# Optimization experiments

Hardware: AMD Instinct MI355X
Metric: run time of the kernel (lower is better)

## Reference

```python
import jax, jax.numpy as jnp
import numpy as np

EMBED_DIM = 1024
NUM_HEADS = 16
HEAD_DIM = EMBED_DIM // NUM_HEADS


def setup_inputs() -> dict:
    key = jax.random.key(0)
    k1, k2, k3, k4, k5 = jax.random.split(key, 5)
    B, N, C = 8, 1024, EMBED_DIM
    s = 1.0 / np.sqrt(C)
    return {
        "x": jax.random.normal(k1, (B, N, C), dtype=jnp.float32),
        "in_proj_weight": jax.random.normal(k2, (3 * C, C), dtype=jnp.float32) * s,
        "in_proj_bias": jax.random.normal(k3, (3 * C,), dtype=jnp.float32) * 0.02,
        "out_proj_weight": jax.random.normal(k4, (C, C), dtype=jnp.float32) * s,
        "out_proj_bias": jax.random.normal(k5, (C,), dtype=jnp.float32) * 0.02,
    }


def reference(x, in_proj_weight, in_proj_bias, out_proj_weight, out_proj_bias):
    B, N, C = x.shape
    scale = HEAD_DIM ** -0.5
    # qkv projection: F.linear(x, W, b) = x @ W.T + b -> [B, N, 3C]
    qkv = jnp.einsum("bnc,dc->bnd", x, in_proj_weight) + in_proj_bias
    # [B, N, 3, H, Dh] -> [3, B, H, N, Dh]
    qkv = qkv.reshape(B, N, 3, NUM_HEADS, HEAD_DIM).transpose(2, 0, 3, 1, 4)
    q, k, v = qkv[0], qkv[1], qkv[2]
    attn = jnp.einsum("bhqd,bhkd->bhqk", q, k) * scale
    attn = jax.nn.softmax(attn, axis=-1)
    out = jnp.einsum("bhqk,bhkd->bhqd", attn, v)
    out = out.transpose(0, 2, 1, 3).reshape(B, N, C)
    return jnp.einsum("bnc,dc->bnd", out, out_proj_weight) + out_proj_bias
```

## Files before the change

### kernel.cpp

```cpp
#include <hip/hip_runtime.h>
#include <math.h>
#include <stdint.h>

#define SEQ   1024
#define BATCH 8
#define CDIM  1024
#define HEADS 16
#define DHEAD 64

typedef __bf16 bf16;
typedef _Float16 f16;
typedef __attribute__((ext_vector_type(8))) __bf16 bf16x8;
typedef __attribute__((ext_vector_type(8))) _Float16 f16x8;
typedef __attribute__((ext_vector_type(4))) float f32x4;

static __device__ __forceinline__ void gl16(const void* g, void* l) {
    __builtin_amdgcn_global_load_lds(
        (const __attribute__((address_space(1))) void*)(uintptr_t)g,
        (__attribute__((address_space(3))) void*)(uintptr_t)l,
        16, 0, 0);
}

__global__ __launch_bounds__(256)
void cvt_f16(const float* __restrict__ in, f16* __restrict__ out, int n8)
{
    int i = blockIdx.x * blockDim.x + threadIdx.x;
    const int stride = gridDim.x * blockDim.x;
    for (; i < n8; i += stride) {
        const f32x4 v0 = *(const f32x4*)(in + (size_t)i * 8);
        const f32x4 v1 = *(const f32x4*)(in + (size_t)i * 8 + 4);
        f16x8 o;
#pragma unroll
        for (int j = 0; j < 4; j++) {
            o[j]     = (f16)v0[j];
            o[j + 4] = (f16)v1[j];
        }
        *(f16x8*)(out + (size_t)i * 8) = o;
    }
}

template<int MODE>
__global__ __launch_bounds__(256, 4)
void gemm_f16(const f16* __restrict__ Ag, const f16* __restrict__ Bg,
              const float* __restrict__ bias, float* __restrict__ out0,
              f16* __restrict__ qg, f16* __restrict__ kgp, f16* __restrict__ vgp,
              int M, int Ncols, int K)
{
    __shared__ f16 As[4][128][8];
    __shared__ f16 Bs[4][128][8];

    const int tid  = threadIdx.x;
    const int m0   = blockIdx.y * 128;
    const int n0   = blockIdx.x * 128;
    const int wid  = tid >> 6;
    const int lane = tid & 63;
    const int wr   = (wid >> 1) * 64;
    const int wc   = (wid & 1) * 64;
    const int l16  = lane & 15;
    const int kgf  = lane >> 4;

    const int kg0 = tid >> 7, row0 = tid & 127;

    const f16* aP = Ag + (size_t)(m0 + row0) * K + kg0 * 8;
    const f16* bP = Bg + (size_t)(n0 + row0) * K + kg0 * 8;

    char* ldsA = (char*)&As[0][0][0] + (wid << 10);
    char* ldsB = (char*)&Bs[0][0][0] + (wid << 10);

    f32x4 acc[4][4];
#pragma unroll
    for (int i = 0; i < 4; i++)
#pragma unroll
        for (int j = 0; j < 4; j++) acc[i][j] = (f32x4)0.f;

    for (int kt = 0; kt < K; kt += 32) {
        __syncthreads();
        gl16(aP + kt,      ldsA);
        gl16(aP + kt + 16, ldsA + 4096);
        gl16(bP + kt,      ldsB);
        gl16(bP + kt + 16, ldsB + 4096);
        __syncthreads();

        f16x8 fa[4], fb[4];
#pragma unroll
        for (int i = 0; i < 4; i++) {
            fa[i] = *(const f16x8*)&As[kgf][wr + i * 16 + l16][0];
            fb[i] = *(const f16x8*)&Bs[kgf][wc + i * 16 + l16][0];
        }
#pragma unroll
        for (int mi = 0; mi < 4; mi++)
#pragma unroll
            for (int ni = 0; ni < 4; ni++)
                acc[mi][ni] = __builtin_amdgcn_mfma_f32_16x16x32_f16(
                    fa[mi], fb[ni], acc[mi][ni], 0, 0, 0);
    }

#pragma unroll
    for (int ni = 0; ni < 4; ni++) {
        const int d  = n0 + wc + ni * 16 + l16;
        const float bv = bias[d];
        int s = 0, hh = 0, dh = 0;
        if (MODE == 1) {
            s  = d >> 10;
            hh = (d >> 6) & 15;
            dh = d & 63;
        }
#pragma unroll
        for (int mi = 0; mi < 4; mi++) {
            const int mbase = m0 + wr + mi * 16 + (lane >> 4) * 4;
#pragma unroll
            for (int r = 0; r < 4; r++) {
                const float v = acc[mi][ni][r] + bv;
                const int m = mbase + r;
                if (MODE == 0) {
                    out0[(size_t)m * Ncols + d] = v;
                } else {
                    const int b = m >> 10, n = m & 1023;
                    const size_t bho = (size_t)((b << 4) + hh) << 16;
                    if (s == 0)
                        qg[bho + ((size_t)n << 6) + dh] = (f16)(v * 0.125f);
                    else if (s == 1)
                        kgp[bho + ((size_t)n << 6) + dh] = (f16)v;
                    else
                        vgp[bho + ((size_t)dh << 10) + n] = (f16)v;
                }
            }
        }
    }
    (void)M;
}

__global__ __launch_bounds__(256, 4)
void attn_mfma(const f16* __restrict__ qf, const f16* __restrict__ kf,
               const f16* __restrict__ vtf, f16* __restrict__ og)
{
    __shared__ f16 Kl[8][64][8];
    __shared__ f16 Vl[8][64][8];
    __shared__ f16 Pl[4][16][72];

    const int tid  = threadIdx.x;
    const int wid  = tid >> 6;
    const int lane = tid & 63;
    const int l16  = lane & 15;
    const int kg   = lane >> 4;
    const int bh   = blockIdx.y;
    const int q0   = blockIdx.x << 6;

    const size_t bhoff = (size_t)bh << 16;
    const f16* qb = qf  + bhoff;
    const f16* kb = kf  + bhoff;
    const f16* vb = vtf + bhoff;

    f16x8 qfr[2];
    {
        const f16* qrow = qb + ((size_t)(q0 + wid * 16 + l16) << 6);
        qfr[0] = *(const f16x8*)(qrow + kg * 8);
        qfr[1] = *(const f16x8*)(qrow + 32 + kg * 8);
    }

    const int c0 = tid,        col0 = c0 & 63, slot0 = c0 >> 6;
    const int c1 = tid + 256,  col1 = c1 & 63, slot1 = c1 >> 6;

    float mrow[4], lrow[4];
    f32x4 accO[4];
#pragma unroll
    for (int r = 0; r < 4; r++) { mrow[r] = -INFINITY; lrow[r] = 0.f; }
#pragma unroll
    for (int t = 0; t < 4; t++) accO[t] = (f32x4)0.f;

    f16x8 rk0 = *(const f16x8*)(kb + ((size_t)col0 << 6) + slot0 * 8);
    f16x8 rk1 = *(const f16x8*)(kb + ((size_t)col1 << 6) + slot1 * 8);
    f16x8 rv0 = *(const f16x8*)(vb + ((size_t)col0 << 10) + slot0 * 8);
    f16x8 rv1 = *(const f16x8*)(vb + ((size_t)col1 << 10) + slot1 * 8);

    for (int kt = 0; kt < 16; kt++) {
        __syncthreads();
        *(f16x8*)&Kl[slot0][col0][0] = rk0;
        *(f16x8*)&Kl[slot1][col1][0] = rk1;
        *(f16x8*)&Vl[slot0][col0][0] = rv0;
        *(f16x8*)&Vl[slot1][col1][0] = rv1;
        __syncthreads();

        if (kt < 15) {
            const int n1 = (kt + 1) << 6;
            rk0 = *(const f16x8*)(kb + ((size_t)(n1 + col0) << 6) + slot0 * 8);
            rk1 = *(const f16x8*)(kb + ((size_t)(n1 + col1) << 6) + slot1 * 8);
            rv0 = *(const f16x8*)(vb + ((size_t)col0 << 10) + n1 + slot0 * 8);
            rv1 = *(const f16x8*)(vb + ((size_t)col1 << 10) + n1 + slot1 * 8);
        }

        f32x4 accS[4];
#pragma unroll
        for (int t = 0; t < 4; t++) accS[t] = (f32x4)0.f;
#pragma unroll
        for (int t = 0; t < 4; t++) {
            const f16x8 kf0 = *(const f16x8*)&Kl[kg][t * 16 + l16][0];
            const f16x8 kf1 = *(const f16x8*)&Kl[4 + kg][t * 16 + l16][0];
            accS[t] = __builtin_amdgcn_mfma_f32_16x16x32_f16(qfr[0], kf0, accS[t], 0, 0, 0);
            accS[t] = __builtin_amdgcn_mfma_f32_16x16x32_f16(qfr[1], kf1, accS[t], 0, 0, 0);
        }

#pragma unroll
        for (int r = 0; r < 4; r++) {
            float sm = fmaxf(fmaxf(accS[0][r], accS[1][r]),
                             fmaxf(accS[2][r], accS[3][r]));
            sm = fmaxf(sm, __shfl_xor(sm, 1, 16));
            sm = fmaxf(sm, __shfl_xor(sm, 2, 16));
            sm = fmaxf(sm, __shfl_xor(sm, 4, 16));
            sm = fmaxf(sm, __shfl_xor(sm, 8, 16));
            const float mn = fmaxf(mrow[r], sm);
            const float al = __expf(mrow[r] - mn);
            float p0 = __expf(accS[0][r] - mn);
            float p1 = __expf(accS[1][r] - mn);
            float p2 = __expf(accS[2][r] - mn);
            float p3 = __expf(accS[3][r] - mn);
            float rs = (p0 + p1) + (p2 + p3);
            rs += __shfl_xor(rs, 1, 16);
            rs += __shfl_xor(rs, 2, 16);
            rs += __shfl_xor(rs, 4, 16);
            rs += __shfl_xor(rs, 8, 16);
            lrow[r] = lrow[r] * al + rs;
            mrow[r] = mn;
            accO[0][r] *= al;
            accO[1][r] *= al;
            accO[2][r] *= al;
            accO[3][r] *= al;
            const int prow = kg * 4 + r;
            Pl[wid][prow][l16]      = (f16)p0;
            Pl[wid][prow][16 + l16] = (f16)p1;
            Pl[wid][prow][32 + l16] = (f16)p2;
            Pl[wid][prow][48 + l16] = (f16)p3;
        }

#pragma unroll
        for (int h = 0; h < 2; h++) {
            const f16x8 pa = *(const f16x8*)&Pl[wid][l16][h * 32 + kg * 8];
#pragma unroll
            for (int t = 0; t < 4; t++) {
                const f16x8 vf = *(const f16x8*)&Vl[h * 4 + kg][t * 16 + l16][0];
                accO[t] = __builtin_amdgcn_mfma_f32_16x16x32_f16(pa, vf, accO[t], 0, 0, 0);
            }
        }
    }

    const int b = bh >> 4, hh = bh & 15;
#pragma unroll
    for (int r = 0; r < 4; r++) {
        const float inv = 1.0f / lrow[r];
        const int n = q0 + wid * 16 + kg * 4 + r;
        const size_t base = ((((size_t)b << 10) + n) << 10) + hh * 64;
#pragma unroll
        for (int t = 0; t < 4; t++)
            og[base + t * 16 + l16] = (f16)(accO[t][r] * inv);
    }
}

#define TILE 128
#define KB   16
#define LSTR (TILE + 4)

template<int MODE>
__global__ __launch_bounds__(256, 2)
void gemm_bt(const float* __restrict__ A, const float* __restrict__ Bm,
             const float* __restrict__ bias, float* __restrict__ out0,
             float* __restrict__ qg, float* __restrict__ kg, float* __restrict__ vg,
             int M, int Ncols, int K)
{
    __shared__ float As[KB][LSTR];
    __shared__ float Bs[KB][LSTR];

    const int tid = threadIdx.x;
    const int tr  = tid >> 4;
    const int tc  = tid & 15;
    const int m0  = blockIdx.y * TILE;
    const int n0  = blockIdx.x * TILE;

    const int lrow = tid >> 2;
    const int lcol = (tid & 3) << 2;

    const float* Ap = A  + (size_t)(m0 + lrow) * K + lcol;
    const float* Bp = Bm + (size_t)(n0 + lrow) * K + lcol;
    const size_t rstep = (size_t)64 * K;

    float acc[8][8];
#pragma unroll
    for (int i = 0; i < 8; i++)
#pragma unroll
        for (int j = 0; j < 8; j++) acc[i][j] = 0.f;

    for (int kt = 0; kt < K; kt += KB) {
        float4 a0 = *(const float4*)(Ap + kt);
        float4 a1 = *(const float4*)(Ap + rstep + kt);
        float4 b0 = *(const float4*)(Bp + kt);
        float4 b1 = *(const float4*)(Bp + rstep + kt);
        __syncthreads();
        As[lcol + 0][lrow]      = a0.x;
        As[lcol + 1][lrow]      = a0.y;
        As[lcol + 2][lrow]      = a0.z;
        As[lcol + 3][lrow]      = a0.w;
        As[lcol + 0][lrow + 64] = a1.x;
        As[lcol + 1][lrow + 64] = a1.y;
        As[lcol + 2][lrow + 64] = a1.z;
        As[lcol + 3][lrow + 64] = a1.w;
        Bs[lcol + 0][lrow]      = b0.x;
        Bs[lcol + 1][lrow]      = b0.y;
        Bs[lcol + 2][lrow]      = b0.z;
        Bs[lcol + 3][lrow]      = b0.w;
        Bs[lcol + 0][lrow + 64] = b1.x;
        Bs[lcol + 1][lrow + 64] = b1.y;
        Bs[lcol + 2][lrow + 64] = b1.z;
        Bs[lcol + 3][lrow + 64] = b1.w;
        __syncthreads();
#pragma unroll
        for (int kk = 0; kk < KB; kk++) {
            float ar[8], br[8];
            *(float4*)&ar[0] = *(const float4*)&As[kk][tr << 2];
            *(float4*)&ar[4] = *(const float4*)&As[kk][64 + (tr << 2)];
            *(float4*)&br[0] = *(const float4*)&Bs[kk][tc << 2];
            *(float4*)&br[4] = *(const float4*)&Bs[kk][64 + (tc << 2)];
#pragma unroll
            for (int i = 0; i < 8; i++)
#pragma unroll
                for (int j = 0; j < 8; j++)
                    acc[i][j] = fmaf(ar[i], br[j], acc[i][j]);
        }
    }

#pragma unroll
    for (int rg = 0; rg < 2; rg++) {
#pragma unroll
        for (int ri = 0; ri < 4; ri++) {
            const int m = m0 + rg * 64 + (tr << 2) + ri;
#pragma unroll
            for (int cg = 0; cg < 2; cg++) {
                const int d = n0 + cg * 64 + (tc << 2);
                const float4 bb = *(const float4*)&bias[d];
                float v0 = acc[rg * 4 + ri][cg * 4 + 0] + bb.x;
                float v1 = acc[rg * 4 + ri][cg * 4 + 1] + bb.y;
                float v2 = acc[rg * 4 + ri][cg * 4 + 2] + bb.z;
                float v3 = acc[rg * 4 + ri][cg * 4 + 3] + bb.w;
                if (MODE == 0) {
                    *(float4*)&out0[(size_t)m * Ncols + d] = make_float4(v0, v1, v2, v3);
                } else {
                    const int s  = d >> 10;
                    const int h  = (d >> 6) & 15;
                    const int dh = d & 63;
                    const int b  = m >> 10;
                    const int n  = m & 1023;
                    float* dst = (s == 0) ? qg : ((s == 1) ? kg : vg);
                    if (s == 0) { v0 *= 0.125f; v1 *= 0.125f; v2 *= 0.125f; v3 *= 0.125f; }
                    const size_t idx = (((size_t)((b << 4) + h) << 10) + n) * 64 + dh;
                    *(float4*)&dst[idx] = make_float4(v0, v1, v2, v3);
                }
            }
        }
    }
}

__global__ __launch_bounds__(256, 2)
void attn_flash_f32(const float* __restrict__ qg, const float* __restrict__ kg,
                    const float* __restrict__ vg, float* __restrict__ og)
{
    __shared__ float Qs[64][68];
    __shared__ float KPs[64][68];
    __shared__ float Vs[64][68];

    const int tid = threadIdx.x;
    const int tr  = tid >> 4;
    const int tc  = tid & 15;
    const int bh  = blockIdx.y;
    const int q0  = blockIdx.x << 6;

    const float* qb = qg + ((size_t)bh * SEQ + q0) * DHEAD;
    const float* kb = kg + (size_t)bh * SEQ * DHEAD;
    const float* vb = vg + (size_t)bh * SEQ * DHEAD;

    const int lr = tid >> 4;
    const int lc = (tid & 15) << 2;

#pragma unroll
    for (int i = 0; i < 4; i++) {
        const int r = lr + (i << 4);
        float4 t = *(const float4*)(qb + r * 64 + lc);
        Qs[lc + 0][r] = t.x;
        Qs[lc + 1][r] = t.y;
        Qs[lc + 2][r] = t.z;
        Qs[lc + 3][r] = t.w;
    }

    float m[4], l[4], acc[4][4];
#pragma unroll
    for (int i = 0; i < 4; i++) {
        m[i] = -INFINITY; l[i] = 0.f;
#pragma unroll
        for (int j = 0; j < 4; j++) acc[i][j] = 0.f;
    }

    for (int kt = 0; kt < 16; kt++) {
        __syncthreads();
        const float* kbt = kb + (size_t)(kt << 6) * 64;
        const float* vbt = vb + (size_t)(kt << 6) * 64;
#pragma unroll
        for (int i = 0; i < 4; i++) {
            const int r = lr + (i << 4);
            float4 t = *(const float4*)(kbt + r * 64 + lc);
            KPs[lc + 0][r] = t.x;
            KPs[lc + 1][r] = t.y;
            KPs[lc + 2][r] = t.z;
            KPs[lc + 3][r] = t.w;
            float4 tv = *(const float4*)(vbt + r * 64 + lc);
            *(float4*)&Vs[r][lc] = tv;
        }
        __syncthreads();

        float s[4][4];
#pragma unroll
        for (int i = 0; i < 4; i++)
#pragma unroll
            for (int j = 0; j < 4; j++) s[i][j] = 0.f;
#pragma unroll 4
        for (int d = 0; d < 64; d++) {
            float qa[4], ka[4];
            *(float4*)qa = *(const float4*)&Qs[d][tr << 2];
            *(float4*)ka = *(const float4*)&KPs[d][tc << 2];
#pragma unroll
            for (int ri = 0; ri < 4; ri++)
#pragma unroll
                for (int ci = 0; ci < 4; ci++)
                    s[ri][ci] = fmaf(qa[ri], ka[ci], s[ri][ci]);
        }
        __syncthreads();

#pragma unroll
        for (int ri = 0; ri < 4; ri++) {
            float tm = fmaxf(fmaxf(s[ri][0], s[ri][1]), fmaxf(s[ri][2], s[ri][3]));
            tm = fmaxf(tm, __shfl_xor(tm, 1, 16));
            tm = fmaxf(tm, __shfl_xor(tm, 2, 16));
            tm = fmaxf(tm, __shfl_xor(tm, 4, 16));
            tm = fmaxf(tm, __shfl_xor(tm, 8, 16));
            const float mn = fmaxf(m[ri], tm);
            const float alpha = __expf(m[ri] - mn);
            const float p0 = __expf(s[ri][0] - mn);
            const float p1 = __expf(s[ri][1] - mn);
            const float p2 = __expf(s[ri][2] - mn);
            const float p3 = __expf(s[ri][3] - mn);
            float rs = (p0 + p1) + (p2 + p3);
            rs += __shfl_xor(rs, 1, 16);
            rs += __shfl_xor(rs, 2, 16);
            rs += __shfl_xor(rs, 4, 16);
            rs += __shfl_xor(rs, 8, 16);
            l[ri] = l[ri] * alpha + rs;
            m[ri] = mn;
            acc[ri][0] *= alpha; acc[ri][1] *= alpha;
            acc[ri][2] *= alpha; acc[ri][3] *= alpha;
            *(float4*)&KPs[(tr << 2) + ri][tc << 2] = make_float4(p0, p1, p2, p3);
        }
        __syncthreads();

#pragma unroll 4
        for (int c = 0; c < 64; c += 4) {
            float pr[4][4], vv[4][4];
            *(float4*)pr[0] = *(const float4*)&KPs[(tr << 2) + 0][c];
            *(float4*)pr[1] = *(const float4*)&KPs[(tr << 2) + 1][c];
            *(float4*)pr[2] = *(const float4*)&KPs[(tr << 2) + 2][c];
            *(float4*)pr[3] = *(const float4*)&KPs[(tr << 2) + 3][c];
            *(float4*)vv[0] = *(const float4*)&Vs[c + 0][tc << 2];
            *(float4*)vv[1] = *(const float4*)&Vs[c + 1][tc << 2];
            *(float4*)vv[2] = *(const float4*)&Vs[c + 2][tc << 2];
            *(float4*)vv[3] = *(const float4*)&Vs[c + 3][tc << 2];
#pragma unroll
            for (int ri = 0; ri < 4; ri++)
#pragma unroll
                for (int j = 0; j < 4; j++) {
                    float a = acc[ri][j];
                    a = fmaf(pr[ri][0], vv[0][j], a);
                    a = fmaf(pr[ri][1], vv[1][j], a);
                    a = fmaf(pr[ri][2], vv[2][j], a);
                    a = fmaf(pr[ri][3], vv[3][j], a);
                    acc[ri][j] = a;
                }
        }
    }

    const int b = bh >> 4, h = bh & 15;
#pragma unroll
    for (int ri = 0; ri < 4; ri++) {
        const float inv = 1.0f / l[ri];
        const int n = q0 + (tr << 2) + ri;
        const size_t idx = (((size_t)b * SEQ + n) << 10) + (h << 6) + (tc << 2);
        *(float4*)&og[idx] = make_float4(acc[ri][0] * inv, acc[ri][1] * inv,
                                         acc[ri][2] * inv, acc[ri][3] * inv);
    }
}

extern "C" void kernel_launch(void* const* d_in, const int* in_sizes, int n_in,
                              void* d_out, int out_size, void* d_ws, size_t ws_size,
                              hipStream_t stream)
{
    const float* x     = (const float*)d_in[0];
    const float* w_in  = (const float*)d_in[1];
    const float* b_in  = (const float*)d_in[2];
    const float* w_out = (const float*)d_in[3];
    const float* b_out = (const float*)d_in[4];
    float* out = (float*)d_out;
    (void)in_sizes; (void)n_in; (void)out_size;

    const size_t MB  = 1024 * 1024;
    const size_t per = (size_t)BATCH * HEADS * SEQ * DHEAD;
    const int    M   = BATCH * SEQ;
    char* ws = (char*)d_ws;

    if (ws_size >= 96 * MB) {
        f16* qf16  = (f16*)(ws + 0 * MB);
        f16* kf16  = (f16*)(ws + 16 * MB);
        f16* vtf16 = (f16*)(ws + 32 * MB);
        f16* xf16  = (f16*)(ws + 48 * MB);
        f16* of16  = xf16;
        f16* wif16 = (f16*)(ws + 64 * MB);
        f16* wof16 = (f16*)(ws + 70 * MB);

        cvt_f16<<<2048, 256, 0, stream>>>(x,     xf16,  (int)(per / 8));
        cvt_f16<<<1024, 256, 0, stream>>>(w_in,  wif16, 3 * CDIM * CDIM / 8);
        cvt_f16<<<512,  256, 0, stream>>>(w_out, wof16, CDIM * CDIM / 8);

        gemm_f16<1><<<dim3(3 * CDIM / 128, M / 128), 256, 0, stream>>>(
            xf16, wif16, b_in, nullptr, qf16, kf16, vtf16, M, 3 * CDIM, CDIM);

        attn_mfma<<<dim3(SEQ / 64, BATCH * HEADS), 256, 0, stream>>>(
            qf16, kf16, vtf16, of16);

        gemm_f16<0><<<dim3(CDIM / 128, M / 128), 256, 0, stream>>>(
            of16, wof16, b_out, out, nullptr, nullptr, nullptr, M, CDIM, CDIM);
    } else {
        float* qws = (float*)d_ws;
        float* kws = qws + per;
        float* vws = kws + per;
        float* aws = vws + per;

        gemm_bt<1><<<dim3(3 * CDIM / TILE, M / TILE), 256, 0, stream>>>(
            x, w_in, b_in, nullptr, qws, kws, vws, M, 3 * CDIM, CDIM);

        attn_flash_f32<<<dim3(SEQ / 64, BATCH * HEADS), 256, 0, stream>>>(
            qws, kws, vws, aws);

        gemm_bt<0><<<dim3(CDIM / TILE, M / TILE), 256, 0, stream>>>(
            aws, w_out, b_out, out, nullptr, nullptr, nullptr, M, CDIM, CDIM);
    }
}
```

Before: 289.0 us.

## Double-buffer GEMM LDS tiles and swizzle workgroup order for L2 locality

Splits the GEMM shared-memory tiles into two buffers so the global-to-LDS loads for the next K step are issued while MFMAs run on the current one, dropping one barrier per iteration. It also remaps the linear workgroup index in groups of eight so neighbouring workgroups share A/B rows in cache. LDS use per block doubles, which may limit occupancy under launch_bounds(256,4), and the swizzle assumes the workgroup count is divisible by eight.

```diff
diff --git a/kernel.cpp b/kernel.cpp
--- a/kernel.cpp
+++ b/kernel.cpp
@@ -10,7 +10,6 @@
 
 typedef __bf16 bf16;
 typedef _Float16 f16;
-typedef __attribute__((ext_vector_type(8))) __bf16 bf16x8;
 typedef __attribute__((ext_vector_type(8))) _Float16 f16x8;
 typedef __attribute__((ext_vector_type(4))) float f32x4;
 
@@ -46,12 +45,18 @@
               f16* __restrict__ qg, f16* __restrict__ kgp, f16* __restrict__ vgp,
               int M, int Ncols, int K)
 {
-    __shared__ f16 As[4][128][8];
-    __shared__ f16 Bs[4][128][8];
+    __shared__ f16 As[2][4][128][8];
+    __shared__ f16 Bs[2][4][128][8];
+
+    const int nx   = gridDim.x;
+    const int nwg  = nx * gridDim.y;
+    const int lin  = blockIdx.y * nx + blockIdx.x;
+    const int cpx  = nwg >> 3;
+    const int swz  = (lin & 7) * cpx + (lin >> 3);
+    const int m0   = (swz / nx) * 128;
+    const int n0   = (swz % nx) * 128;
 
     const int tid  = threadIdx.x;
-    const int m0   = blockIdx.y * 128;
-    const int n0   = blockIdx.x * 128;
     const int wid  = tid >> 6;
     const int lane = tid & 63;
     const int wr   = (wid >> 1) * 64;
@@ -60,12 +65,9 @@
     const int kgf  = lane >> 4;
 
     const int kg0 = tid >> 7, row0 = tid & 127;
-
     const f16* aP = Ag + (size_t)(m0 + row0) * K + kg0 * 8;
     const f16* bP = Bg + (size_t)(n0 + row0) * K + kg0 * 8;
-
-    char* ldsA = (char*)&As[0][0][0] + (wid << 10);
-    char* ldsB = (char*)&Bs[0][0][0] + (wid << 10);
+    const int loff = wid << 10;
 
     f32x4 acc[4][4];
 #pragma unroll
@@ -73,19 +75,29 @@
 #pragma unroll
         for (int j = 0; j < 4; j++) acc[i][j] = (f32x4)0.f;
 
-    for (int kt = 0; kt < K; kt += 32) {
-        __syncthreads();
-        gl16(aP + kt,      ldsA);
-        gl16(aP + kt + 16, ldsA + 4096);
-        gl16(bP + kt,      ldsB);
-        gl16(bP + kt + 16, ldsB + 4096);
-        __syncthreads();
+    gl16(aP,      (char*)&As[0][0][0][0] + loff);
+    gl16(aP + 16, (char*)&As[0][0][0][0] + loff + 4096);
+    gl16(bP,      (char*)&Bs[0][0][0][0] + loff);
+    gl16(bP + 16, (char*)&Bs[0][0][0][0] + loff + 4096);
+    __syncthreads();
+
+    const int T = K >> 5;
+    for (int t = 0; t < T; t++) {
+        const int cur = t & 1;
+        if (t + 1 < T) {
+            const int nxt = cur ^ 1;
+            const int kn  = (t + 1) << 5;
+            gl16(aP + kn,      (char*)&As[nxt][0][0][0] + loff);
+            gl16(aP + kn + 16, (char*)&As[nxt][0][0][0] + loff + 4096);
+            gl16(bP + kn,      (char*)&Bs[nxt][0][0][0] + loff);
+            gl16(bP + kn + 16, (char*)&Bs[nxt][0][0][0] + loff + 4096);
+        }
 
         f16x8 fa[4], fb[4];
 #pragma unroll
         for (int i = 0; i < 4; i++) {
-            fa[i] = *(const f16x8*)&As[kgf][wr + i * 16 + l16][0];
-            fb[i] = *(const f16x8*)&Bs[kgf][wc + i * 16 + l16][0];
+            fa[i] = *(const f16x8*)&As[cur][kgf][wr + i * 16 + l16][0];
+            fb[i] = *(const f16x8*)&Bs[cur][kgf][wc + i * 16 + l16][0];
         }
 #pragma unroll
         for (int mi = 0; mi < 4; mi++)
@@ -93,6 +105,8 @@
             for (int ni = 0; ni < 4; ni++)
                 acc[mi][ni] = __builtin_amdgcn_mfma_f32_16x16x32_f16(
                     fa[mi], fb[ni], acc[mi][ni], 0, 0, 0);
+
+        __syncthreads();
     }
 
 #pragma unroll
```

After: 285.4 us. About the same (-1.2%).

## Triple-buffer GEMM LDS tiles with async prefetch two stages ahead

Applied to the files above, without the earlier changes.

Replaces the single-buffer load-sync-compute loop in the f16 GEMM with a three-stage LDS ring. Direct global-to-LDS loads are issued two K-tiles ahead, and explicit vmcnt waits plus barriers gate each compute step. The goal is to hide global memory latency behind the MFMA work instead of stalling on every tile. In exchange, LDS per block triples, and the occupancy hint drops from 4 to 3 blocks per CU.

```diff
diff --git a/kernel.cpp b/kernel.cpp
--- a/kernel.cpp
+++ b/kernel.cpp
@@ -10,7 +10,6 @@
 
 typedef __bf16 bf16;
 typedef _Float16 f16;
-typedef __attribute__((ext_vector_type(8))) __bf16 bf16x8;
 typedef __attribute__((ext_vector_type(8))) _Float16 f16x8;
 typedef __attribute__((ext_vector_type(4))) float f32x4;
 
@@ -40,18 +39,19 @@
 }
 
 template<int MODE>
-__global__ __launch_bounds__(256, 4)
+__global__ __launch_bounds__(256, 3)
 void gemm_f16(const f16* __restrict__ Ag, const f16* __restrict__ Bg,
               const float* __restrict__ bias, float* __restrict__ out0,
               f16* __restrict__ qg, f16* __restrict__ kgp, f16* __restrict__ vgp,
               int M, int Ncols, int K)
 {
-    __shared__ f16 As[4][128][8];
-    __shared__ f16 Bs[4][128][8];
-
-    const int tid  = threadIdx.x;
+    __shared__ f16 As[3][4][128][8];
+    __shared__ f16 Bs[3][4][128][8];
+
     const int m0   = blockIdx.y * 128;
     const int n0   = blockIdx.x * 128;
+
+    const int tid  = threadIdx.x;
     const int wid  = tid >> 6;
     const int lane = tid & 63;
     const int wr   = (wid >> 1) * 64;
@@ -60,12 +60,33 @@
     const int kgf  = lane >> 4;
 
     const int kg0 = tid >> 7, row0 = tid & 127;
-
     const f16* aP = Ag + (size_t)(m0 + row0) * K + kg0 * 8;
     const f16* bP = Bg + (size_t)(n0 + row0) * K + kg0 * 8;
-
-    char* ldsA = (char*)&As[0][0][0] + (wid << 10);
-    char* ldsB = (char*)&Bs[0][0][0] + (wid << 10);
+    const int loff = wid << 10;
+
+#define STAGE(buf, kt)                                              \
+    do {                                                            \
+        gl16(aP + (kt),      (char*)&As[buf][0][0][0] + loff);      \
+        gl16(aP + (kt) + 16, (char*)&As[buf][0][0][0] + loff + 4096);\
+        gl16(bP + (kt),      (char*)&Bs[buf][0][0][0] + loff);      \
+        gl16(bP + (kt) + 16, (char*)&Bs[buf][0][0][0] + loff + 4096);\
+    } while (0)
+
+#define COMPUTE(buf)                                                        \
+    do {                                                                    \
+        f16x8 fa[4], fb[4];                                                 \
+        _Pragma("unroll")                                                   \
+        for (int i = 0; i < 4; i++) {                                       \
+            fa[i] = *(const f16x8*)&As[buf][kgf][wr + i * 16 + l16][0];     \
+            fb[i] = *(const f16x8*)&Bs[buf][kgf][wc + i * 16 + l16][0];     \
+        }                                                                   \
+        _Pragma("unroll")                                                   \
+        for (int mi = 0; mi < 4; mi++)                                      \
+            _Pragma("unroll")                                               \
+            for (int ni = 0; ni < 4; ni++)                                  \
+                acc[mi][ni] = __builtin_amdgcn_mfma_f32_16x16x32_f16(       \
+                    fa[mi], fb[ni], acc[mi][ni], 0, 0, 0);                  \
+    } while (0)
 
     f32x4 acc[4][4];
 #pragma unroll
@@ -73,27 +94,42 @@
 #pragma unroll
         for (int j = 0; j < 4; j++) acc[i][j] = (f32x4)0.f;
 
-    for (int kt = 0; kt < K; kt += 32) {
-        __syncthreads();
-        gl16(aP + kt,      ldsA);
-        gl16(aP + kt + 16, ldsA + 4096);
-        gl16(bP + kt,      ldsB);
-        gl16(bP + kt + 16, ldsB + 4096);
-        __syncthreads();
-
-        f16x8 fa[4], fb[4];
-#pragma unroll
-        for (int i = 0; i < 4; i++) {
-            fa[i] = *(const f16x8*)&As[kgf][wr + i * 16 + l16][0];
-            fb[i] = *(const f16x8*)&Bs[kgf][wc + i * 16 + l16][0];
-        }
-#pragma unroll
-        for (int mi = 0; mi < 4; mi++)
-#pragma unroll
-            for (int ni = 0; ni < 4; ni++)
-                acc[mi][ni] = __builtin_amdgcn_mfma_f32_16x16x32_f16(
-                    fa[mi], fb[ni], acc[mi][ni], 0, 0, 0);
-    }
+    const int T = K >> 5;
+
+    STAGE(0, 0);
+    STAGE(1, 32);
+
+    int cur = 0;
+    for (int t = 0; t < T - 2; t++) {
+        const int nbuf = (cur == 0) ? 2 : (cur - 1);
+        STAGE(nbuf, (t + 2) << 5);
+        asm volatile("s_waitcnt vmcnt(8)" ::: "memory");
+        __builtin_amdgcn_sched_barrier(0);
+        __builtin_amdgcn_s_barrier();
+        __builtin_amdgcn_sched_barrier(0);
+        COMPUTE(cur);
+        __builtin_amdgcn_sched_barrier(0);
+        __builtin_amdgcn_s_barrier();
+        cur = (cur == 2) ? 0 : (cur + 1);
+    }
+
+    asm volatile("s_waitcnt vmcnt(4)" ::: "memory");
+    __builtin_amdgcn_sched_barrier(0);
+    __builtin_amdgcn_s_barrier();
+    __builtin_amdgcn_sched_barrier(0);
+    COMPUTE(cur);
+    __builtin_amdgcn_sched_barrier(0);
+    __builtin_amdgcn_s_barrier();
+    cur = (cur == 2) ? 0 : (cur + 1);
+
+    asm volatile("s_waitcnt vmcnt(0)" ::: "memory");
+    __builtin_amdgcn_sched_barrier(0);
+    __builtin_amdgcn_s_barrier();
+    __builtin_amdgcn_sched_barrier(0);
+    COMPUTE(cur);
+
+#undef STAGE
+#undef COMPUTE
 
 #pragma unroll
     for (int ni = 0; ni < 4; ni++) {
```

Measured after the change: 286.9 us. About the same (-0.7%).

## Double-buffer GEMM with 128x256 tiles and merge conversion kernels

Applied to the files above, without the earlier changes.

The GEMM now uses 128x256 output tiles per block, so each wave computes a 64x128 sub-tile. The K-loop prefetches the next K-slice into a second LDS buffer with async global-to-LDS loads and waits only on the older loads before computing. The three fp32-to-fp16 conversion launches become one kernel. This cuts the per-iteration load-latency stall and launch overhead. In exchange it uses more registers and LDS, with occupancy lowered to 3 waves, and the output projection now runs only 256 blocks, which may underfill the GPU.

```diff
diff --git a/kernel.cpp b/kernel.cpp
--- a/kernel.cpp
+++ b/kernel.cpp
@@ -10,7 +10,6 @@
 
 typedef __bf16 bf16;
 typedef _Float16 f16;
-typedef __attribute__((ext_vector_type(8))) __bf16 bf16x8;
 typedef __attribute__((ext_vector_type(8))) _Float16 f16x8;
 typedef __attribute__((ext_vector_type(4))) float f32x4;
 
@@ -22,82 +21,117 @@
 }
 
 __global__ __launch_bounds__(256)
-void cvt_f16(const float* __restrict__ in, f16* __restrict__ out, int n8)
+void cvt_all(const float* __restrict__ x,  const float* __restrict__ wi,
+             const float* __restrict__ wo, f16* __restrict__ xo,
+             f16* __restrict__ wio, f16* __restrict__ woo)
 {
+    const int N1 = 1048576, N2 = 393216;
+    const int NT = N1 + N2 + 131072;
     int i = blockIdx.x * blockDim.x + threadIdx.x;
     const int stride = gridDim.x * blockDim.x;
-    for (; i < n8; i += stride) {
-        const f32x4 v0 = *(const f32x4*)(in + (size_t)i * 8);
-        const f32x4 v1 = *(const f32x4*)(in + (size_t)i * 8 + 4);
+    for (; i < NT; i += stride) {
+        const float* src; f16* dst; int off;
+        if (i < N1)            { src = x;  dst = xo;  off = i; }
+        else if (i < N1 + N2)  { src = wi; dst = wio; off = i - N1; }
+        else                   { src = wo; dst = woo; off = i - N1 - N2; }
+        const f32x4 v0 = *(const f32x4*)(src + (size_t)off * 8);
+        const f32x4 v1 = *(const f32x4*)(src + (size_t)off * 8 + 4);
         f16x8 o;
 #pragma unroll
         for (int j = 0; j < 4; j++) {
             o[j]     = (f16)v0[j];
             o[j + 4] = (f16)v1[j];
         }
-        *(f16x8*)(out + (size_t)i * 8) = o;
+        *(f16x8*)(dst + (size_t)off * 8) = o;
     }
 }
 
 template<int MODE>
-__global__ __launch_bounds__(256, 4)
-void gemm_f16(const f16* __restrict__ Ag, const f16* __restrict__ Bg,
-              const float* __restrict__ bias, float* __restrict__ out0,
-              f16* __restrict__ qg, f16* __restrict__ kgp, f16* __restrict__ vgp,
-              int M, int Ncols, int K)
+__global__ __launch_bounds__(256, 3)
+void gemm_wide(const f16* __restrict__ Ag, const f16* __restrict__ Bg,
+               const float* __restrict__ bias, float* __restrict__ out0,
+               f16* __restrict__ qg, f16* __restrict__ kgp,
+               f16* __restrict__ vgp, int Ncols, int K)
 {
-    __shared__ f16 As[4][128][8];
-    __shared__ f16 Bs[4][128][8];
+    __shared__ f16 As[2][4][128][8];
+    __shared__ f16 Bs[2][4][256][8];
+
+    const int m0 = blockIdx.y * 128;
+    const int n0 = blockIdx.x * 256;
 
     const int tid  = threadIdx.x;
-    const int m0   = blockIdx.y * 128;
-    const int n0   = blockIdx.x * 128;
     const int wid  = tid >> 6;
     const int lane = tid & 63;
     const int wr   = (wid >> 1) * 64;
-    const int wc   = (wid & 1) * 64;
+    const int wc   = (wid & 1) * 128;
     const int l16  = lane & 15;
     const int kgf  = lane >> 4;
 
-    const int kg0 = tid >> 7, row0 = tid & 127;
-
-    const f16* aP = Ag + (size_t)(m0 + row0) * K + kg0 * 8;
-    const f16* bP = Bg + (size_t)(n0 + row0) * K + kg0 * 8;
-
-    char* ldsA = (char*)&As[0][0][0] + (wid << 10);
-    char* ldsB = (char*)&Bs[0][0][0] + (wid << 10);
-
-    f32x4 acc[4][4];
+    const int akg = tid >> 7, arow = tid & 127;
+    const f16* aP = Ag + (size_t)(m0 + arow) * K + akg * 8;
+    const f16* bP = Bg + (size_t)(n0 + tid) * K;
+    const int loff = wid << 10;
+
+#define STAGE(buf, kt)                                               \
+    do {                                                             \
+        gl16(aP + (kt),      (char*)As[buf] + loff);                 \
+        gl16(aP + (kt) + 16, (char*)As[buf] + loff + 4096);          \
+        gl16(bP + (kt),      (char*)Bs[buf] + loff);                 \
+        gl16(bP + (kt) + 8,  (char*)Bs[buf] + loff + 4096);         \
+        gl16(bP + (kt) + 16, (char*)Bs[buf] + loff + 8192);         \
+        gl16(bP + (kt) + 24, (char*)Bs[buf] + loff + 12288);        \
+    } while (0)
+
+#define COMPUTE(buf)                                                         \
+    do {                                                                     \
+        f16x8 fa[4], fb[8];                                                  \
+        _Pragma("unroll")                                                    \
+        for (int i = 0; i < 4; i++)                                          \
+            fa[i] = *(const f16x8*)&As[buf][kgf][wr + i * 16 + l16][0];      \
+        _Pragma("unroll")                                                    \
+        for (int j = 0; j < 8; j++)                                          \
+            fb[j] = *(const f16x8*)&Bs[buf][kgf][wc + j * 16 + l16][0];      \
+        _Pragma("unroll")                                                    \
+        for (int i = 0; i < 4; i++)                                          \
+            _Pragma("unroll")                                                \
+            for (int j = 0; j < 8; j++)                                      \
+                acc[i][j] = __builtin_amdgcn_mfma_f32_16x16x32_f16(          \
+                    fa[i], fb[j], acc[i][j], 0, 0, 0);                       \
+    } while (0)
+
+    f32x4 acc[4][8];
 #pragma unroll
     for (int i = 0; i < 4; i++)
 #pragma unroll
-        for (int j = 0; j < 4; j++) acc[i][j] = (f32x4)0.f;
-
-    for (int kt = 0; kt < K; kt += 32) {
-        __syncthreads();
-        gl16(aP + kt,      ldsA);
-        gl16(aP + kt + 16, ldsA + 4096);
-        gl16(bP + kt,      ldsB);
-        gl16(bP + kt + 16, ldsB + 4096);
-        __syncthreads();
-
-        f16x8 fa[4], fb[4];
-#pragma unroll
-        for (int i = 0; i < 4; i++) {
-            fa[i] = *(const f16x8*)&As[kgf][wr + i * 16 + l16][0];
-            fb[i] = *(const f16x8*)&Bs[kgf][wc + i * 16 + l16][0];
-        }
-#pragma unroll
-        for (int mi = 0; mi < 4; mi++)
-#pragma unroll
-            for (int ni = 0; ni < 4; ni++)
-                acc[mi][ni] = __builtin_amdgcn_mfma_f32_16x16x32_f16(
-                    fa[mi], fb[ni], acc[mi][ni], 0, 0, 0);
-    }
-
-#pragma unroll
-    for (int ni = 0; ni < 4; ni++) {
-        const int d  = n0 + wc + ni * 16 + l16;
+        for (int j = 0; j < 8; j++) acc[i][j] = (f32x4)0.f;
+
+    const int T = K >> 5;
+
+    STAGE(0, 0);
+
+    int cur = 0;
+    for (int t = 0; t < T; t++) {
+        if (t + 1 < T) {
+            STAGE(cur ^ 1, (t + 1) << 5);
+            asm volatile("s_waitcnt vmcnt(6)" ::: "memory");
+        } else {
+            asm volatile("s_waitcnt vmcnt(0)" ::: "memory");
+        }
+        __builtin_amdgcn_sched_barrier(0);
+        __builtin_amdgcn_s_barrier();
+        __builtin_amdgcn_sched_barrier(0);
+        COMPUTE(cur);
+        __builtin_amdgcn_sched_barrier(0);
+        __builtin_amdgcn_s_barrier();
+        cur ^= 1;
+    }
+
+#undef STAGE
+#undef COMPUTE
+
+#pragma unroll
+    for (int j = 0; j < 8; j++) {
+        const int d  = n0 + wc + j * 16 + l16;
         const float bv = bias[d];
         int s = 0, hh = 0, dh = 0;
         if (MODE == 1) {
@@ -106,11 +140,11 @@
             dh = d & 63;
         }
 #pragma unroll
-        for (int mi = 0; mi < 4; mi++) {
-            const int mbase = m0 + wr + mi * 16 + (lane >> 4) * 4;
+        for (int i = 0; i < 4; i++) {
+            const int mbase = m0 + wr + i * 16 + (lane >> 4) * 4;
 #pragma unroll
             for (int r = 0; r < 4; r++) {
-                const float v = acc[mi][ni][r] + bv;
+                const float v = acc[i][j][r] + bv;
                 const int m = mbase + r;
                 if (MODE == 0) {
                     out0[(size_t)m * Ncols + d] = v;
@@ -127,7 +161,6 @@
             }
         }
     }
-    (void)M;
 }
 
 __global__ __launch_bounds__(256, 4)
@@ -519,18 +552,16 @@
         f16* wif16 = (f16*)(ws + 64 * MB);
         f16* wof16 = (f16*)(ws + 70 * MB);
 
-        cvt_f16<<<2048, 256, 0, stream>>>(x,     xf16,  (int)(per / 8));
-        cvt_f16<<<1024, 256, 0, stream>>>(w_in,  wif16, 3 * CDIM * CDIM / 8);
-        cvt_f16<<<512,  256, 0, stream>>>(w_out, wof16, CDIM * CDIM / 8);
-
-        gemm_f16<1><<<dim3(3 * CDIM / 128, M / 128), 256, 0, stream>>>(
-            xf16, wif16, b_in, nullptr, qf16, kf16, vtf16, M, 3 * CDIM, CDIM);
+        cvt_all<<<1536, 256, 0, stream>>>(x, w_in, w_out, xf16, wif16, wof16);
+
+        gemm_wide<1><<<dim3(3 * CDIM / 256, M / 128), 256, 0, stream>>>(
+            xf16, wif16, b_in, nullptr, qf16, kf16, vtf16, 3 * CDIM, CDIM);
 
         attn_mfma<<<dim3(SEQ / 64, BATCH * HEADS), 256, 0, stream>>>(
             qf16, kf16, vtf16, of16);
 
-        gemm_f16<0><<<dim3(CDIM / 128, M / 128), 256, 0, stream>>>(
-            of16, wof16, b_out, out, nullptr, nullptr, nullptr, M, CDIM, CDIM);
+        gemm_wide<0><<<dim3(CDIM / 256, M / 128), 256, 0, stream>>>(
+            of16, wof16, b_out, out, nullptr, nullptr, nullptr, CDIM, CDIM);
     } else {
         float* qws = (float*)d_ws;
         float* kws = qws + per;
```

Result: slower. 310.9 us (+7.6%).
